# Kernel optimization log

Hardware: AMD Instinct MI355X
Metric: run time of the kernel (lower is better)

The kernel has to match this reference:

```python
import jax, jax.numpy as jnp
import numpy as np

D_MODEL, D_STATE, D_CONV, EXPAND = 1024, 16, 4, 2
D_INNER = EXPAND * D_MODEL
B, L = 2, 2048
DT = 0.1  # module hard-codes dt = 0.1 (dt_proj is unused)


def setup_inputs() -> dict:
    key = jax.random.key(0)
    ks = jax.random.split(key, 7)
    s = 0.02
    x = jax.random.normal(ks[0], (B, L, D_MODEL), dtype=jnp.float32)
    in_proj_w = jax.random.normal(ks[1], (2 * D_INNER, D_MODEL), dtype=jnp.float32) * s
    conv_w = jax.random.normal(ks[2], (D_INNER, 1, D_CONV), dtype=jnp.float32) * s
    conv_b = jnp.zeros((D_INNER,), dtype=jnp.float32)
    x_proj_w = jax.random.normal(ks[3], (2 * D_STATE, D_INNER), dtype=jnp.float32) * s
    A_log = jnp.log(jnp.tile(jnp.arange(1, D_STATE + 1, dtype=jnp.float32), (D_INNER, 1)))
    D_param = jnp.ones((D_INNER,), dtype=jnp.float32)
    out_proj_w = jax.random.normal(ks[4], (D_MODEL, D_INNER), dtype=jnp.float32) * s
    return {"x": x, "in_proj_w": in_proj_w, "conv_w": conv_w, "conv_b": conv_b,
            "x_proj_w": x_proj_w, "A_log": A_log, "D_param": D_param,
            "out_proj_w": out_proj_w}


def _silu(v):
    return v * jax.nn.sigmoid(v)


def reference(x, in_proj_w, conv_w, conv_b, x_proj_w, A_log, D_param, out_proj_w):
    # in_proj: (B,L,d_model) -> (B,L,2*d_inner)
    xz = jnp.einsum('bld,ed->ble', x, in_proj_w)
    xs, z = jnp.split(xz, 2, axis=-1)
    # depthwise causal conv1d (torch pads both sides d_conv-1 then slices [:L] == left-pad only)
    xc = jax.lax.conv_general_dilated(
        xs.transpose(0, 2, 1), conv_w, window_strides=(1,),
        padding=[(D_CONV - 1, 0)], dimension_numbers=('NCH', 'OIH', 'NCH'),
        feature_group_count=D_INNER) + conv_b[None, :, None]
    xs = _silu(xc.transpose(0, 2, 1))  # (B, L, d_inner)
    # x_proj -> B_proj, C_proj  (B,L,d_state) each
    x_dbl = jnp.einsum('bld,ed->ble', xs, x_proj_w)
    B_proj, C_proj = jnp.split(x_dbl, 2, axis=-1)
    # SSM scan; dt is constant 0.1 so dA = exp(dt*A) is time-invariant
    A = -jnp.exp(A_log)                 # (d_inner, d_state)
    dA = jnp.exp(DT * A)                # (d_inner, d_state)

    def step(h, inp):
        x_t, B_t, C_t = inp             # (B,D), (B,N), (B,N)
        h = dA[None] * h + DT * B_t[:, None, :] * x_t[:, :, None]
        y_t = jnp.einsum('bdn,bn->bd', h, C_t)
        return h, y_t

    h0 = jnp.zeros((B, D_INNER, D_STATE), dtype=xs.dtype)
    _, ys = jax.lax.scan(step, h0,
                         (xs.transpose(1, 0, 2), B_proj.transpose(1, 0, 2), C_proj.transpose(1, 0, 2)))
    y = ys.transpose(1, 0, 2) + xs * D_param[None, None, :]
    y = y * _silu(z)
    return jnp.einsum('bld,ed->ble', y, out_proj_w)
```

## Files before the change

kernel.cpp:

```cpp
#include <hip/hip_runtime.h>
#include <hip/hip_bf16.h>
#include <math.h>

#define D_MODEL 1024
#define D_STATE 16
#define D_CONV  4
#define D_INNER 2048
#define BATCH   2
#define SEQ     2048
#define M_TOTAL (BATCH*SEQ)
#define DT_VAL  0.1f

#define CHUNK 64
#define WARM  64
#define NCHUNK (SEQ / CHUNK)
#define TSTEP 8

typedef __attribute__((ext_vector_type(8))) __bf16 bf16x8;
typedef __attribute__((ext_vector_type(4))) __bf16 bf16x4;
typedef __attribute__((ext_vector_type(4))) float floatx4;

__device__ __forceinline__ void gld_lds16(const __bf16* g, __bf16* l) {
    __builtin_amdgcn_global_load_lds(
        (const __attribute__((address_space(1))) void*)g,
        (__attribute__((address_space(3))) void*)l, 16, 0, 0);
}

template<int EPI, int LDA, int LDW, int KLEN, int NBX>
__global__ __launch_bounds__(256) void gemm_v5(
    const __bf16* __restrict__ A, const __bf16* __restrict__ W,
    float* __restrict__ Cf, float* __restrict__ Cf2, int ldc,
    __bf16* __restrict__ O1, __bf16* __restrict__ O2)
{
    __shared__ __bf16 As[2][128][32];
    __shared__ __bf16 Bs[2][128][32];

    const int tid  = threadIdx.x;
    const int bid  = blockIdx.x;
    const int xcd  = bid & 7;
    const int i    = bid >> 3;
    const int byl  = i & 3;
    const int rest = i >> 2;
    const int bx   = rest % NBX;
    const int ks   = rest / NBX;
    const int m0   = (xcd * 4 + byl) * 128;
    const int n0   = bx * 128;
    const int koff = ks * KLEN;

    const int wave = tid >> 6;
    const int lane = tid & 63;
    const int wr   = (wave >> 1) << 6;
    const int wc   = (wave & 1) << 6;
    const int fm   = lane & 15;
    const int fk   = (lane >> 4) << 3;
    const int grow = lane >> 2;
    const int gcol = (lane & 3) << 3;
    const int arow = wave * 16 + grow;

    floatx4 acc[4][4];
    #pragma unroll
    for (int a = 0; a < 4; ++a)
        #pragma unroll
        for (int b = 0; b < 4; ++b)
            acc[a][b] = (floatx4){0.f, 0.f, 0.f, 0.f};

    const __bf16* ap = A + (size_t)(m0 + arow) * LDA + koff + gcol;
    const __bf16* wp = W + (size_t)(n0 + arow) * LDW + koff + gcol;

    for (int k0 = 0; k0 < KLEN; k0 += 64) {
        __syncthreads();
        #pragma unroll
        for (int p = 0; p < 2; ++p) {
            gld_lds16(ap + k0 + p * 32,                    &As[p][arow][gcol]);
            gld_lds16(ap + k0 + p * 32 + (size_t)64 * LDA, &As[p][arow + 64][gcol]);
            gld_lds16(wp + k0 + p * 32,                    &Bs[p][arow][gcol]);
            gld_lds16(wp + k0 + p * 32 + (size_t)64 * LDW, &Bs[p][arow + 64][gcol]);
        }
        __syncthreads();

        #pragma unroll
        for (int p = 0; p < 2; ++p) {
            bf16x8 af[4], bfv[4];
            #pragma unroll
            for (int a = 0; a < 4; ++a)
                af[a] = *(bf16x8*)&As[p][wr + a * 16 + fm][fk];
            #pragma unroll
            for (int b = 0; b < 4; ++b)
                bfv[b] = *(bf16x8*)&Bs[p][wc + b * 16 + fm][fk];
            #pragma unroll
            for (int a = 0; a < 4; ++a)
                #pragma unroll
                for (int b = 0; b < 4; ++b)
                    acc[a][b] = __builtin_amdgcn_mfma_f32_16x16x32_bf16(
                        af[a], bfv[b], acc[a][b], 0, 0, 0);
        }
    }

    const int crow = (lane >> 4) << 2;
    const int ccol = lane & 15;
    #pragma unroll
    for (int a = 0; a < 4; ++a) {
        #pragma unroll
        for (int b = 0; b < 4; ++b) {
            const int cm = m0 + wr + a * 16 + crow;
            const int cn = n0 + wc + b * 16 + ccol;
            #pragma unroll
            for (int r = 0; r < 4; ++r) {
                const float v = acc[a][b][r];
                if (EPI == 1) {
                    if (n0 < 2048) {
                        O1[(size_t)(cm + r) * 2048 + cn] = (__bf16)v;
                    } else {
                        const float s = v / (1.f + __expf(-v));
                        O2[(size_t)(cm + r) * 2048 + cn - 2048] = (__bf16)s;
                    }
                } else {
                    float* dst = (ks < 2 ? Cf : Cf2) +
                                 (size_t)(ks & 1) * M_TOTAL * ldc;
                    dst[(size_t)(cm + r) * ldc + cn] = v;
                }
            }
        }
    }
}

__global__ __launch_bounds__(256) void reduce4(
    const float* __restrict__ p01, const float* __restrict__ p23,
    float* __restrict__ out)
{
    const size_t i = (size_t)(blockIdx.x * 256 + threadIdx.x) * 4;
    const float4 a = *(const float4*)(p01 + i);
    const float4 b = *(const float4*)(p01 + (size_t)M_TOTAL * D_MODEL + i);
    const float4 c = *(const float4*)(p23 + i);
    const float4 d = *(const float4*)(p23 + (size_t)M_TOTAL * D_MODEL + i);
    float4 o;
    o.x = (a.x + b.x) + (c.x + d.x);
    o.y = (a.y + b.y) + (c.y + d.y);
    o.z = (a.z + b.z) + (c.z + d.z);
    o.w = (a.w + b.w) + (c.w + d.w);
    *(float4*)(out + i) = o;
}

__global__ __launch_bounds__(256) void xproj_mfma(
    const __bf16* __restrict__ X, const __bf16* __restrict__ Wp,
    float* __restrict__ bc)
{
    __shared__ __bf16 Ash[128][32];
    __shared__ __bf16 Wsh[32][264];

    const int tid  = threadIdx.x;
    const int bid  = blockIdx.x;
    const int ks   = bid & 7;
    const int mb   = bid >> 3;
    const int m0   = mb * 128;
    const int koff = ks * 256;
    const int wave = tid >> 6;
    const int lane = tid & 63;
    const int fm   = lane & 15;
    const int fk   = (lane >> 4) << 3;
    const int grow = lane >> 2;
    const int gcol = (lane & 3) << 3;

    {
        const int r = tid >> 3;
        const int c = (tid & 7) << 5;
        #pragma unroll
        for (int q = 0; q < 4; ++q)
            *(bf16x8*)&Wsh[r][c + q * 8] =
                *(const bf16x8*)(Wp + (size_t)r * D_INNER + koff + c + q * 8);
    }

    floatx4 acc[2][2];
    #pragma unroll
    for (int a = 0; a < 2; ++a)
        #pragma unroll
        for (int b = 0; b < 2; ++b)
            acc[a][b] = (floatx4){0.f, 0.f, 0.f, 0.f};

    for (int kit = 0; kit < 8; ++kit) {
        const int kg = koff + kit * 32;
        __syncthreads();
        #pragma unroll
        for (int issue = 0; issue < 2; ++issue) {
            const int r = issue * 64 + wave * 16 + grow;
            gld_lds16(X + (size_t)(m0 + r) * D_INNER + kg + gcol, &Ash[r][gcol]);
        }
        __syncthreads();

        bf16x8 af[2], wf[2];
        af[0] = *(bf16x8*)&Ash[wave * 32 + fm][fk];
        af[1] = *(bf16x8*)&Ash[wave * 32 + 16 + fm][fk];
        wf[0] = *(bf16x8*)&Wsh[fm][kit * 32 + fk];
        wf[1] = *(bf16x8*)&Wsh[16 + fm][kit * 32 + fk];
        #pragma unroll
        for (int a = 0; a < 2; ++a)
            #pragma unroll
            for (int b = 0; b < 2; ++b)
                acc[a][b] = __builtin_amdgcn_mfma_f32_16x16x32_bf16(
                    af[a], wf[b], acc[a][b], 0, 0, 0);
    }

    const int crow = (lane >> 4) << 2;
    const int ccol = lane & 15;
    #pragma unroll
    for (int a = 0; a < 2; ++a)
        #pragma unroll
        for (int b = 0; b < 2; ++b)
            #pragma unroll
            for (int r = 0; r < 4; ++r)
                atomicAdd(bc + (size_t)(m0 + wave * 32 + a * 16 + crow + r) * 32
                             + b * 16 + ccol, acc[a][b][r]);
}

__global__ __launch_bounds__(256) void cast5(
    const float* __restrict__ x, const float* __restrict__ win,
    const float* __restrict__ wout, const float* __restrict__ xpw,
    __bf16* __restrict__ xbf, __bf16* __restrict__ winbf,
    __bf16* __restrict__ woutbf, __bf16* __restrict__ xpwbf,
    float* __restrict__ bcz)
{
    const size_t g = (size_t)(blockIdx.x * 256 + threadIdx.x);
    if (g >= 2637824) {
        const size_t off = (g - 2637824) * 4;
        *(float4*)(bcz + off) = (float4){0.f, 0.f, 0.f, 0.f};
        return;
    }
    const size_t j = g * 4;
    const float* src; __bf16* dst; size_t off;
    if (j < 4194304)       { src = x;    dst = xbf;    off = j; }
    else if (j < 8388608)  { src = win;  dst = winbf;  off = j - 4194304; }
    else if (j < 10485760) { src = wout; dst = woutbf; off = j - 8388608; }
    else                   { src = xpw;  dst = xpwbf;  off = j - 10485760; }
    const float4 v = *(const float4*)(src + off);
    bf16x4 o;
    o[0] = (__bf16)v.x; o[1] = (__bf16)v.y; o[2] = (__bf16)v.z; o[3] = (__bf16)v.w;
    *(bf16x4*)(dst + off) = o;
}

__global__ __launch_bounds__(256) void conv_silu4(
    const __bf16* __restrict__ xsp, const float* __restrict__ cw,
    const float* __restrict__ cb, __bf16* __restrict__ xsc)
{
    const int g    = blockIdx.x * 256 + threadIdx.x;
    const int d4   = g & (D_INNER / 4 - 1);
    const int mblk = g >> 9;
    const int m0   = mblk << 2;
    const int d    = d4 << 2;

    const float4 w0 = *(const float4*)(cw + (size_t)(d + 0) * 4);
    const float4 w1 = *(const float4*)(cw + (size_t)(d + 1) * 4);
    const float4 w2 = *(const float4*)(cw + (size_t)(d + 2) * 4);
    const float4 w3 = *(const float4*)(cw + (size_t)(d + 3) * 4);
    const float4 bv = *(const float4*)(cb + d);

    float4 rows[7];
    const int lbase = m0 & (SEQ - 1);
    #pragma unroll
    for (int j = 0; j < 7; ++j) {
        if (lbase + j >= 3) {
            const bf16x4 v = *(const bf16x4*)(xsp + (size_t)(m0 + j - 3) * D_INNER + d);
            rows[j].x = (float)v[0]; rows[j].y = (float)v[1];
            rows[j].z = (float)v[2]; rows[j].w = (float)v[3];
        } else {
            rows[j] = (float4){0.f, 0.f, 0.f, 0.f};
        }
    }

    #pragma unroll
    for (int o = 0; o < 4; ++o) {
        float a0 = bv.x, a1 = bv.y, a2 = bv.z, a3 = bv.w;
        #pragma unroll
        for (int j = 0; j < 4; ++j) {
            const float4 v = rows[o + j];
            const float wj0 = (j==0)?w0.x:(j==1)?w0.y:(j==2)?w0.z:w0.w;
            const float wj1 = (j==0)?w1.x:(j==1)?w1.y:(j==2)?w1.z:w1.w;
            const float wj2 = (j==0)?w2.x:(j==1)?w2.y:(j==2)?w2.z:w2.w;
            const float wj3 = (j==0)?w3.x:(j==1)?w3.y:(j==2)?w3.z:w3.w;
            a0 = fmaf(wj0, v.x, a0);
            a1 = fmaf(wj1, v.y, a1);
            a2 = fmaf(wj2, v.z, a2);
            a3 = fmaf(wj3, v.w, a3);
        }
        a0 = a0 / (1.f + __expf(-a0));
        a1 = a1 / (1.f + __expf(-a1));
        a2 = a2 / (1.f + __expf(-a2));
        a3 = a3 / (1.f + __expf(-a3));
        bf16x4 ob;
        ob[0] = (__bf16)a0; ob[1] = (__bf16)a1;
        ob[2] = (__bf16)a2; ob[3] = (__bf16)a3;
        *(bf16x4*)(xsc + (size_t)(m0 + o) * D_INNER + d) = ob;
    }
}

__global__ __launch_bounds__(256) void ssm_scan(
    const __bf16* __restrict__ xsc, const float* __restrict__ bc,
    const __bf16* __restrict__ szbf, __bf16* __restrict__ ybf,
    const float* __restrict__ alog, const float* __restrict__ dpar)
{
    __shared__ float Bsh[CHUNK + WARM][16];
    __shared__ float Csh[CHUNK + WARM][16];
    __shared__ float Xsh[2][TSTEP][256];
    __shared__ float Zsh[2][TSTEP][256];

    const int tid = threadIdx.x;
    const int blk = blockIdx.x;
    const int db  = blk & 7;
    const int ch  = (blk >> 3) & (NCHUNK - 1);
    const int b   = blk >> 8;
    const int d0  = db * 256;
    const int d   = d0 + tid;
    const int t0  = ch * CHUNK;
    const int tw  = (t0 >= WARM) ? (t0 - WARM) : 0;
    const int warm = t0 - tw;
    const int nt  = t0 + CHUNK - tw;
    const int ntiles = nt / TSTEP;

    const float* bcp = bc + ((size_t)b * SEQ + tw) * 32;
    for (int i = tid; i < nt * 8; i += 256) {
        const int row = i >> 3, q = i & 7;
        const float4 v = *(const float4*)(bcp + (size_t)row * 32 + q * 4);
        if (q < 4) *(float4*)&Bsh[row][q * 4] = v;
        else       *(float4*)&Csh[row][(q - 4) * 4] = v;
    }

    float dAv[16], h[16];
    #pragma unroll
    for (int q = 0; q < 4; ++q) {
        const float4 av = *(const float4*)(alog + (size_t)d * D_STATE + q * 4);
        dAv[q*4+0] = expf(-DT_VAL * expf(av.x));
        dAv[q*4+1] = expf(-DT_VAL * expf(av.y));
        dAv[q*4+2] = expf(-DT_VAL * expf(av.z));
        dAv[q*4+3] = expf(-DT_VAL * expf(av.w));
    }
    #pragma unroll
    for (int n = 0; n < 16; ++n) h[n] = 0.f;
    const float Dd = dpar[d];

    const __bf16* xbase = xsc  + ((size_t)b * SEQ + tw) * D_INNER + d0;
    const __bf16* zbase = szbf + ((size_t)b * SEQ + tw) * D_INNER + d0;
    __bf16*       ybase = ybf  + ((size_t)b * SEQ + tw) * D_INNER + d0;

    const int lrow = tid >> 6;
    const int lcol = (tid & 63) << 2;

    {
        const bf16x4 xa = *(const bf16x4*)(xbase + (size_t)lrow * D_INNER + lcol);
        const bf16x4 xb = *(const bf16x4*)(xbase + (size_t)(lrow + 4) * D_INNER + lcol);
        float4 fa, fb;
        fa.x=(float)xa[0]; fa.y=(float)xa[1]; fa.z=(float)xa[2]; fa.w=(float)xa[3];
        fb.x=(float)xb[0]; fb.y=(float)xb[1]; fb.z=(float)xb[2]; fb.w=(float)xb[3];
        *(float4*)&Xsh[0][lrow][lcol]     = fa;
        *(float4*)&Xsh[0][lrow + 4][lcol] = fb;
        if (warm == 0) {
            const bf16x4 za = *(const bf16x4*)(zbase + (size_t)lrow * D_INNER + lcol);
            const bf16x4 zb = *(const bf16x4*)(zbase + (size_t)(lrow + 4) * D_INNER + lcol);
            float4 ga, gb;
            ga.x=(float)za[0]; ga.y=(float)za[1]; ga.z=(float)za[2]; ga.w=(float)za[3];
            gb.x=(float)zb[0]; gb.y=(float)zb[1]; gb.z=(float)zb[2]; gb.w=(float)zb[3];
            *(float4*)&Zsh[0][lrow][lcol]     = ga;
            *(float4*)&Zsh[0][lrow + 4][lcol] = gb;
        }
    }
    __syncthreads();

    for (int tile = 0; tile < ntiles; ++tile) {
        const int buf = tile & 1;
        const int s   = tile * TSTEP;
        const int s2  = s + TSTEP;
        const bool more = (tile + 1 < ntiles);
        const bool znext = more && (s2 >= warm);

        bf16x4 rx0, rx1, rz0, rz1;
        if (more) {
            rx0 = *(const bf16x4*)(xbase + (size_t)(s2 + lrow) * D_INNER + lcol);
            rx1 = *(const bf16x4*)(xbase + (size_t)(s2 + lrow + 4) * D_INNER + lcol);
        }
        if (znext) {
            rz0 = *(const bf16x4*)(zbase + (size_t)(s2 + lrow) * D_INNER + lcol);
            rz1 = *(const bf16x4*)(zbase + (size_t)(s2 + lrow + 4) * D_INNER + lcol);
        }

        #pragma unroll
        for (int tt = 0; tt < TSTEP; ++tt) {
            const int t = s + tt;
            const float x   = Xsh[buf][tt][tid];
            const float dtx = DT_VAL * x;
            float y0 = 0.f, y1 = 0.f, y2 = 0.f, y3 = 0.f;
            #pragma unroll
            for (int n = 0; n < 4; ++n) {
                h[n]      = fmaf(dAv[n],      h[n],      dtx * Bsh[t][n]);
                h[n + 4]  = fmaf(dAv[n + 4],  h[n + 4],  dtx * Bsh[t][n + 4]);
                h[n + 8]  = fmaf(dAv[n + 8],  h[n + 8],  dtx * Bsh[t][n + 8]);
                h[n + 12] = fmaf(dAv[n + 12], h[n + 12], dtx * Bsh[t][n + 12]);
                y0 = fmaf(h[n],      Csh[t][n],      y0);
                y1 = fmaf(h[n + 4],  Csh[t][n + 4],  y1);
                y2 = fmaf(h[n + 8],  Csh[t][n + 8],  y2);
                y3 = fmaf(h[n + 12], Csh[t][n + 12], y3);
            }
            if (t >= warm) {
                const float sz = Zsh[buf][tt][tid];
                const float y  = fmaf(x, Dd, (y0 + y1) + (y2 + y3));
                ybase[(size_t)t * D_INNER + tid] = (__bf16)(y * sz);
            }
        }

        if (more) {
            float4 fa, fb;
            fa.x=(float)rx0[0]; fa.y=(float)rx0[1]; fa.z=(float)rx0[2]; fa.w=(float)rx0[3];
            fb.x=(float)rx1[0]; fb.y=(float)rx1[1]; fb.z=(float)rx1[2]; fb.w=(float)rx1[3];
            *(float4*)&Xsh[buf ^ 1][lrow][lcol]     = fa;
            *(float4*)&Xsh[buf ^ 1][lrow + 4][lcol] = fb;
        }
        if (znext) {
            float4 ga, gb;
            ga.x=(float)rz0[0]; ga.y=(float)rz0[1]; ga.z=(float)rz0[2]; ga.w=(float)rz0[3];
            gb.x=(float)rz1[0]; gb.y=(float)rz1[1]; gb.z=(float)rz1[2]; gb.w=(float)rz1[3];
            *(float4*)&Zsh[buf ^ 1][lrow][lcol]     = ga;
            *(float4*)&Zsh[buf ^ 1][lrow + 4][lcol] = gb;
        }
        __syncthreads();
    }
}

extern "C" void kernel_launch(void* const* d_in, const int* in_sizes, int n_in,
                              void* d_out, int out_size, void* d_ws, size_t ws_size,
                              hipStream_t stream)
{
    const float* x    = (const float*)d_in[0];
    const float* win  = (const float*)d_in[1];
    const float* cw   = (const float*)d_in[2];
    const float* cb   = (const float*)d_in[3];
    const float* xpw  = (const float*)d_in[4];
    const float* alog = (const float*)d_in[5];
    const float* dpar = (const float*)d_in[6];
    const float* wout = (const float*)d_in[7];
    float* out = (float*)d_out;

    char* w = (char*)d_ws;
    float*  pbuf   = (float*)w;
    __bf16* szbf   = (__bf16*)(w + 33554432);
    __bf16* xspbf  = (__bf16*)(w + 50331648);
    __bf16* xsc    = (__bf16*)(w + 67108864);
    float*  pbuf2  = (float*)(w + 50331648);
    float*  bcbuf  = (float*)(w + 83886080);
    __bf16* r1     = (__bf16*)(w + 84410368);
    __bf16* xbf    = r1;
    __bf16* winbf  = r1 + 4194304;
    __bf16* ybf    = r1;
    __bf16* woutbf = (__bf16*)(w + 101187584);
    __bf16* xpwbf  = (__bf16*)(w + 105381888);

    cast5<<<10432, 256, 0, stream>>>(x, win, wout, xpw,
                                     xbf, winbf, woutbf, xpwbf, bcbuf);
    gemm_v5<1, 1024, 1024, 1024, 32><<<1024, 256, 0, stream>>>(
        xbf, winbf, nullptr, nullptr, 0, xspbf, szbf);
    conv_silu4<<<(M_TOTAL / 4 * (D_INNER / 4)) / 256, 256, 0, stream>>>(
        xspbf, cw, cb, xsc);
    xproj_mfma<<<256, 256, 0, stream>>>(xsc, xpwbf, bcbuf);
    ssm_scan<<<BATCH * NCHUNK * 8, 256, 0, stream>>>(
        xsc, bcbuf, szbf, ybf, alog, dpar);
    gemm_v5<2, 2048, 2048, 512, 8><<<1024, 256, 0, stream>>>(
        ybf, woutbf, pbuf, pbuf2, D_MODEL, nullptr, nullptr);
    reduce4<<<(M_TOTAL * D_MODEL / 4) / 256, 256, 0, stream>>>(pbuf, pbuf2, out);
}
```

Baseline: 241.8 us.

## Replace in_proj GEMM with 256x256-tile, 8-wave, 4-stage pipelined MFMA kernel

Adds a dedicated in_proj kernel that uses 256x256 output tiles, 512 threads (8 waves), and a 4-buffer LDS ring fed by direct global-to-LDS loads. A and B stages are interleaved with MFMA phases, and s_setprio raises priority around the compute. The goal is more operand reuse per loaded byte and better overlap of loads with MFMA than the 128x128 gemm_v5. In exchange it uses 128KB of LDS and a large accumulator set per thread, which limits occupancy, and the epilogue does uncoalesced scalar bf16 stores.

```diff
diff --git a/kernel.cpp b/kernel.cpp
--- a/kernel.cpp
+++ b/kernel.cpp
@@ -24,6 +24,134 @@
     __builtin_amdgcn_global_load_lds(
         (const __attribute__((address_space(1))) void*)g,
         (__attribute__((address_space(3))) void*)l, 16, 0, 0);
+}
+
+__global__ __launch_bounds__(512, 2) void inproj_8p(
+    const __bf16* __restrict__ A, const __bf16* __restrict__ W,
+    __bf16* __restrict__ O1, __bf16* __restrict__ O2)
+{
+    __shared__ __bf16 As[4][256][32];
+    __shared__ __bf16 Bs[4][256][32];
+    constexpr int LDA = 1024;
+    constexpr int NT  = 1024 / 32;
+
+    const int tid = threadIdx.x;
+    const int bid = blockIdx.x;
+    const int xcd = bid & 7;
+    const int idx = bid >> 3;
+    const int mt  = xcd * 2 + (idx >> 4);
+    const int nt  = idx & 15;
+    const int m0  = mt * 256;
+    const int n0  = nt * 256;
+
+    const int wave = tid >> 6;
+    const int lane = tid & 63;
+    const int wr   = (wave >> 2) * 128;
+    const int wc   = (wave & 3) * 64;
+    const int fm   = lane & 15;
+    const int coff = (((lane >> 4) ^ ((fm >> 1) & 3)) << 3);
+
+    const int srow = tid >> 2;
+    const int sc   = tid & 3;
+    const int sgc  = sc ^ ((srow >> 1) & 3);
+    const __bf16* ga = A + (size_t)(m0 + srow) * LDA + sgc * 8;
+    const __bf16* gb = W + (size_t)(n0 + srow) * LDA + sgc * 8;
+    __bf16* la = &As[0][srow][sc * 8];
+    __bf16* lb = &Bs[0][srow][sc * 8];
+    const size_t rstep = (size_t)128 * LDA;
+
+    const __bf16* fa0 = &As[0][wr + fm][0] + coff;
+    const __bf16* fb0 = &Bs[0][wc + fm][0] + coff;
+
+    floatx4 acc[8][4];
+    #pragma unroll
+    for (int a = 0; a < 8; ++a)
+        #pragma unroll
+        for (int b = 0; b < 4; ++b)
+            acc[a][b] = (floatx4){0.f, 0.f, 0.f, 0.f};
+
+#define STAGE_A(u) { const int _b = (u) & 3; const int _k = (u) * 32;          \
+        gld_lds16(ga + _k,         la + _b * 8192);                            \
+        gld_lds16(ga + _k + rstep, la + _b * 8192 + 4096); }
+#define STAGE_B(u) { const int _b = (u) & 3; const int _k = (u) * 32;          \
+        gld_lds16(gb + _k,         lb + _b * 8192);                            \
+        gld_lds16(gb + _k + rstep, lb + _b * 8192 + 4096); }
+
+    STAGE_A(0); STAGE_B(0);
+    STAGE_A(1); STAGE_B(1);
+    STAGE_A(2); STAGE_B(2);
+    asm volatile("s_waitcnt vmcnt(8)" ::: "memory");
+    __builtin_amdgcn_s_barrier();
+
+    #pragma unroll 4
+    for (int t = 0; t < NT; ++t) {
+        const int cur = t & 3;
+        const __bf16* fA = fa0 + cur * 8192;
+        const __bf16* fB = fb0 + cur * 8192;
+        bf16x8 bfr[4], afr[4];
+
+        #pragma unroll
+        for (int b = 0; b < 4; ++b) bfr[b] = *(const bf16x8*)(fB + b * 512);
+        #pragma unroll
+        for (int a = 0; a < 4; ++a) afr[a] = *(const bf16x8*)(fA + a * 512);
+        if (t + 3 < NT) STAGE_A(t + 3);
+        asm volatile("" ::: "memory");
+        __builtin_amdgcn_s_barrier();
+        __builtin_amdgcn_s_setprio(1);
+        #pragma unroll
+        for (int a = 0; a < 4; ++a)
+            #pragma unroll
+            for (int b = 0; b < 4; ++b)
+                acc[a][b] = __builtin_amdgcn_mfma_f32_16x16x32_bf16(
+                    afr[a], bfr[b], acc[a][b], 0, 0, 0);
+        __builtin_amdgcn_s_setprio(0);
+
+        #pragma unroll
+        for (int a = 0; a < 4; ++a) afr[a] = *(const bf16x8*)(fA + (4 + a) * 512);
+        if (t + 3 < NT) STAGE_B(t + 3);
+        asm volatile("" ::: "memory");
+        __builtin_amdgcn_s_barrier();
+        __builtin_amdgcn_s_setprio(1);
+        #pragma unroll
+        for (int a = 0; a < 4; ++a)
+            #pragma unroll
+            for (int b = 0; b < 4; ++b)
+                acc[4 + a][b] = __builtin_amdgcn_mfma_f32_16x16x32_bf16(
+                    afr[a], bfr[b], acc[4 + a][b], 0, 0, 0);
+        __builtin_amdgcn_s_setprio(0);
+
+        if (t < NT - 3) {
+            asm volatile("s_waitcnt vmcnt(8)" ::: "memory");
+        } else if (t == NT - 3) {
+            asm volatile("s_waitcnt vmcnt(4)" ::: "memory");
+        } else if (t == NT - 2) {
+            asm volatile("s_waitcnt vmcnt(0)" ::: "memory");
+        }
+        if (t < NT - 1) __builtin_amdgcn_s_barrier();
+    }
+#undef STAGE_A
+#undef STAGE_B
+
+    const int crow = (lane >> 4) << 2;
+    const int ccol = lane & 15;
+    #pragma unroll
+    for (int a = 0; a < 8; ++a) {
+        #pragma unroll
+        for (int b = 0; b < 4; ++b) {
+            const int cm = m0 + wr + a * 16 + crow;
+            const int cn = n0 + wc + b * 16 + ccol;
+            #pragma unroll
+            for (int r = 0; r < 4; ++r) {
+                const float v = acc[a][b][r];
+                if (n0 < 2048) {
+                    O1[(size_t)(cm + r) * 2048 + cn] = (__bf16)v;
+                } else {
+                    const float s = v / (1.f + __expf(-v));
+                    O2[(size_t)(cm + r) * 2048 + cn - 2048] = (__bf16)s;
+                }
+            }
+        }
+    }
 }
 
 template<int EPI, int LDA, int LDW, int KLEN, int NBX>
@@ -452,8 +580,7 @@
 
     cast5<<<10432, 256, 0, stream>>>(x, win, wout, xpw,
                                      xbf, winbf, woutbf, xpwbf, bcbuf);
-    gemm_v5<1, 1024, 1024, 1024, 32><<<1024, 256, 0, stream>>>(
-        xbf, winbf, nullptr, nullptr, 0, xspbf, szbf);
+    inproj_8p<<<256, 512, 0, stream>>>(xbf, winbf, xspbf, szbf);
     conv_silu4<<<(M_TOTAL / 4 * (D_INNER / 4)) / 256, 256, 0, stream>>>(
         xspbf, cw, cb, xsc);
     xproj_mfma<<<256, 256, 0, stream>>>(xsc, xpwbf, bcbuf);
```

New measurement: 235.4 us. 2.6% less time.
